# Kernel optimization log

Measured on AMD Instinct MI355X. Metric: run time of the kernel, lower is better.

The kernel has to match this reference:

```python
import jax, jax.numpy as jnp
import numpy as np

B, S, D_MODEL = 4, 2048, 1024
NUM_HEADS, HEAD_DIM = 16, 64
EPS = 1e-6


def setup_inputs() -> dict:
    key = jax.random.key(0)
    ks = jax.random.split(key, 6)
    hd = NUM_HEADS * HEAD_DIM
    scale_in = 1.0 / np.sqrt(D_MODEL)
    scale_hd = 1.0 / np.sqrt(hd)
    return {
        "x": jax.random.normal(ks[0], (B, S, D_MODEL), dtype=jnp.float32),
        "w_q": jax.random.normal(ks[1], (D_MODEL, hd), dtype=jnp.float32) * scale_in,
        "w_k": jax.random.normal(ks[2], (D_MODEL, hd), dtype=jnp.float32) * scale_in,
        "w_v": jax.random.normal(ks[3], (D_MODEL, hd), dtype=jnp.float32) * scale_in,
        "w_proj": jax.random.normal(ks[4], (hd, D_MODEL), dtype=jnp.float32) * scale_hd,
        "b_proj": jax.random.normal(ks[5], (D_MODEL,), dtype=jnp.float32) * 0.01,
        "ln_gamma": jnp.ones((D_MODEL,), dtype=jnp.float32),
        "ln_beta": jnp.zeros((D_MODEL,), dtype=jnp.float32),
    }


def reference(x, w_q, w_k, w_v, w_proj, b_proj, ln_gamma, ln_beta):
    # x: [B, S, D]; project and split heads -> [B, H, S, Dh]
    def split_heads(t):
        b, s, _ = t.shape
        return t.reshape(b, s, NUM_HEADS, HEAD_DIM).transpose(0, 2, 1, 3)

    q = split_heads(x @ w_q)
    k = split_heads(x @ w_k)
    v = split_heads(x @ w_v)

    scale = HEAD_DIM ** (-0.5)
    attn = jnp.einsum("bnqd,bnkd->bnqk", q, k) * scale  # [B, H, S, S]
    attn = jax.nn.softmax(attn, axis=-1)
    o = jnp.einsum("bnqk,bnkd->bnqd", attn, v)  # [B, H, S, Dh]
    o = o.transpose(0, 2, 1, 3).reshape(x.shape[0], x.shape[1], NUM_HEADS * HEAD_DIM)

    # proj + residual (dropout = identity in eval) then LayerNorm(eps=1e-6)
    y = o @ w_proj + b_proj + x
    mean = jnp.mean(y, axis=-1, keepdims=True)
    var = jnp.var(y, axis=-1, keepdims=True)
    y = (y - mean) * jax.lax.rsqrt(var + EPS) * ln_gamma + ln_beta
    return y
```

## Files before the change

### kernel.cpp

```cpp
#include <hip/hip_runtime.h>
#include <hip/hip_fp16.h>


typedef unsigned short u16;
typedef __attribute__((ext_vector_type(8))) u16 u16x8;
typedef __attribute__((ext_vector_type(4))) u16 u16x4;
typedef __attribute__((ext_vector_type(8))) __bf16 bf16x8;
typedef __attribute__((ext_vector_type(4))) _Float16 f16x4;
typedef __attribute__((ext_vector_type(2))) _Float16 f16x2;
typedef __attribute__((ext_vector_type(2))) __fp16 hf16x2;
typedef __attribute__((ext_vector_type(4))) float f32x4;

#define SM_C1 0.1803368801111204f

static __device__ __forceinline__ u16 f2bf(float f) {
  union { float f; unsigned int u; } v; v.f = f;
  unsigned int u = v.u;
  return (u16)((u + 0x7fffu + ((u >> 16) & 1u)) >> 16);
}
static __device__ __forceinline__ u16 f2h(float f) {
  union { _Float16 h; u16 u; } v; v.h = (_Float16)f;
  return v.u;
}

static __device__ __forceinline__ void gld16(const u16* g, u16* l) {
  __builtin_amdgcn_global_load_lds((const __attribute__((address_space(1))) void*)g,
                                   (__attribute__((address_space(3))) void*)l, 16, 0, 0);
}


__global__ __launch_bounds__(256) void k_convx(const float* __restrict__ x,
                                               u16* __restrict__ xbf) {
  int i = (blockIdx.x * 256 + threadIdx.x) * 8;
  float4 a = *(const float4*)(x + i);
  float4 b = *(const float4*)(x + i + 4);
  u16x8 o;
  o[0] = f2bf(a.x); o[1] = f2bf(a.y); o[2] = f2bf(a.z); o[3] = f2bf(a.w);
  o[4] = f2bf(b.x); o[5] = f2bf(b.y); o[6] = f2bf(b.z); o[7] = f2bf(b.w);
  *(u16x8*)(xbf + i) = o;
}

__global__ __launch_bounds__(256) void k_convwT(const float* __restrict__ w0,
                                                const float* __restrict__ w1,
                                                const float* __restrict__ w2,
                                                const float* __restrict__ w3,
                                                u16* __restrict__ o0, u16* __restrict__ o1,
                                                u16* __restrict__ o2, u16* __restrict__ o3) {
  __shared__ float tile[64][65];
  const float* w = blockIdx.z == 0 ? w0 : blockIdx.z == 1 ? w1 : blockIdx.z == 2 ? w2 : w3;
  u16* o = blockIdx.z == 0 ? o0 : blockIdx.z == 1 ? o1 : blockIdx.z == 2 ? o2 : o3;
  const int k0 = blockIdx.x * 64, n0 = blockIdx.y * 64;
  const int t = threadIdx.x;
#pragma unroll
  for (int i = 0; i < 16; i++) {
    int idx = t + 256 * i;
    int k = idx >> 6, n = idx & 63;
    tile[k][n] = w[(k0 + k) * 1024 + n0 + n];
  }
  __syncthreads();
#pragma unroll
  for (int i = 0; i < 16; i++) {
    int idx = t + 256 * i;
    int n = idx >> 6, k = idx & 63;
    o[(n0 + n) * 1024 + k0 + k] = f2bf(tile[k][n]);
  }
}


__global__ __launch_bounds__(256) void k_gemm_qkv(const u16* __restrict__ xbf,
                                                  const u16* __restrict__ wT,
                                                  u16* __restrict__ Qb, u16* __restrict__ Kb,
                                                  u16* __restrict__ VbT) {
  __shared__ alignas(16) u16 Als[128 * 64];
  __shared__ alignas(16) u16 Bls[128 * 64];
  const int t = threadIdx.x;
  const int wv = t >> 6, lane = t & 63, quad = lane >> 4, l16 = lane & 15;
  const int wm = wv >> 1, wn = wv & 1;
  const int m0 = blockIdx.x * 128;
  const int nt = blockIdx.y;
  const int row = t >> 3;
  const int kg = (t & 7) ^ (row & 7);
  const u16* aG = xbf + (size_t)(m0 + row) * 1024 + kg * 8;
  const u16* bG = wT + (size_t)(nt * 128 + row) * 1024 + kg * 8;
  const int sw = l16 & 7;
  const int aA0 = (wm * 64 + l16) * 64 + ((quad) ^ sw) * 8;
  const int aA1 = (wm * 64 + l16) * 64 + ((4 + quad) ^ sw) * 8;
  const int bA0 = (wn * 64 + l16) * 64 + ((quad) ^ sw) * 8;
  const int bA1 = (wn * 64 + l16) * 64 + ((4 + quad) ^ sw) * 8;

  f32x4 acc[4][4] = {};
  for (int k0 = 0; k0 < 1024; k0 += 64) {
    __syncthreads();
#pragma unroll
    for (int i = 0; i < 4; i++) {
      gld16(aG + i * 32 * 1024 + k0, &Als[(i * 256 + wv * 64) * 8]);
      gld16(bG + i * 32 * 1024 + k0, &Bls[(i * 256 + wv * 64) * 8]);
    }
    __syncthreads();
#pragma unroll
    for (int c = 0; c < 2; c++) {
      bf16x8 a[4], b[4];
#pragma unroll
      for (int f = 0; f < 4; f++) a[f] = *(const bf16x8*)&Als[(c ? aA1 : aA0) + f * 1024];
#pragma unroll
      for (int g = 0; g < 4; g++) b[g] = *(const bf16x8*)&Bls[(c ? bA1 : bA0) + g * 1024];
#pragma unroll
      for (int f = 0; f < 4; f++)
#pragma unroll
        for (int g = 0; g < 4; g++)
          acc[f][g] = __builtin_amdgcn_mfma_f32_16x16x32_bf16(a[f], b[g], acc[f][g], 0, 0, 0);
    }
  }

  const int sel = nt >> 3;
  const int n0 = (nt & 7) * 128 + wn * 64;
  const int mBase = m0 + wm * 64 + quad * 4;
  if (sel < 2) {
    u16* Ob = sel == 0 ? Qb : Kb;
    const float scl = sel == 0 ? SM_C1 : 1.0f;
#pragma unroll
    for (int f = 0; f < 4; f++)
#pragma unroll
      for (int g = 0; g < 4; g++)
#pragma unroll
        for (int r = 0; r < 4; r++) {
          int m = mBase + f * 16 + r;
          int n = n0 + g * 16 + l16;
          Ob[(size_t)m * 1024 + n] = f2bf(acc[f][g][r] * scl);
        }
  } else {
#pragma unroll
    for (int f = 0; f < 4; f++) {
      int m = mBase + f * 16;
      int bb = m >> 11, s = m & 2047;
#pragma unroll
      for (int g = 0; g < 4; g++) {
        int n = n0 + g * 16 + l16;
        int hh = n >> 6, dh = n & 63;
        u16x4 o;
#pragma unroll
        for (int r = 0; r < 4; r++) o[r] = f2h(acc[f][g][r]);
        *(u16x4*)&VbT[(size_t)(((bb << 4) + hh) * 64 + dh) * 2048 + s] = o;
      }
    }
  }
}


__global__ __launch_bounds__(256) void k_gemm_proj(const u16* __restrict__ Abf,
                                                   const u16* __restrict__ wT,
                                                   const float* __restrict__ x,
                                                   const float* __restrict__ bias,
                                                   float* __restrict__ ypre) {
  __shared__ alignas(16) u16 Als[128 * 64];
  __shared__ alignas(16) u16 Bls[128 * 64];
  const int t = threadIdx.x;
  const int wv = t >> 6, lane = t & 63, quad = lane >> 4, l16 = lane & 15;
  const int wm = wv >> 1, wn = wv & 1;
  const int m0 = blockIdx.x * 128;
  const int n0t = blockIdx.y * 128;
  const int row = t >> 3;
  const int kg = (t & 7) ^ (row & 7);
  const u16* aG = Abf + (size_t)(m0 + row) * 1024 + kg * 8;
  const u16* bG = wT + (size_t)(n0t + row) * 1024 + kg * 8;
  const int sw = l16 & 7;
  const int aA0 = (wm * 64 + l16) * 64 + ((quad) ^ sw) * 8;
  const int aA1 = (wm * 64 + l16) * 64 + ((4 + quad) ^ sw) * 8;
  const int bA0 = (wn * 64 + l16) * 64 + ((quad) ^ sw) * 8;
  const int bA1 = (wn * 64 + l16) * 64 + ((4 + quad) ^ sw) * 8;

  f32x4 acc[4][4] = {};
  for (int k0 = 0; k0 < 1024; k0 += 64) {
    __syncthreads();
#pragma unroll
    for (int i = 0; i < 4; i++) {
      gld16(aG + i * 32 * 1024 + k0, &Als[(i * 256 + wv * 64) * 8]);
      gld16(bG + i * 32 * 1024 + k0, &Bls[(i * 256 + wv * 64) * 8]);
    }
    __syncthreads();
#pragma unroll
    for (int c = 0; c < 2; c++) {
      bf16x8 a[4], b[4];
#pragma unroll
      for (int f = 0; f < 4; f++) a[f] = *(const bf16x8*)&Als[(c ? aA1 : aA0) + f * 1024];
#pragma unroll
      for (int g = 0; g < 4; g++) b[g] = *(const bf16x8*)&Bls[(c ? bA1 : bA0) + g * 1024];
#pragma unroll
      for (int f = 0; f < 4; f++)
#pragma unroll
        for (int g = 0; g < 4; g++)
          acc[f][g] = __builtin_amdgcn_mfma_f32_16x16x32_bf16(a[f], b[g], acc[f][g], 0, 0, 0);
    }
  }

  const int n0 = n0t + wn * 64;
  const int mBase = m0 + wm * 64 + quad * 4;
#pragma unroll
  for (int g = 0; g < 4; g++) {
    int n = n0 + g * 16 + l16;
    float bn = bias[n];
#pragma unroll
    for (int f = 0; f < 4; f++)
#pragma unroll
      for (int r = 0; r < 4; r++) {
        int m = mBase + f * 16 + r;
        ypre[(size_t)m * 1024 + n] = acc[f][g][r] + bn + x[(size_t)m * 1024 + n];
      }
  }
}


__global__ __launch_bounds__(256) void k_attn(const u16* __restrict__ Qb,
                                              const u16* __restrict__ Kb,
                                              const u16* __restrict__ VbT,
                                              u16* __restrict__ Ob) {
  __shared__ alignas(16) u16 Kls[2][64 * 72];
  __shared__ alignas(16) u16 Vls[2][64 * 72];
  const int b = blockIdx.y >> 4, h = blockIdx.y & 15;
  const int q0 = blockIdx.x * 128;
  const int t = threadIdx.x;
  const int wave = t >> 6, lane = t & 63, quad = lane >> 4, l16 = lane & 15;
  const int sr = t >> 2, sc = (t & 3) * 8;

  bf16x8 aq[2][2];
#pragma unroll
  for (int qf = 0; qf < 2; qf++)
#pragma unroll
    for (int c = 0; c < 2; c++)
      aq[qf][c] = *(const bf16x8*)&Qb[(size_t)(b * 2048 + q0 + wave * 32 + qf * 16 + l16) * 1024 +
                                      h * 64 + c * 32 + quad * 8];

  f32x4 Oacc[2][4] = {};
  float psum[2] = {};

  const u16* kBase = Kb + (size_t)(b * 2048) * 1024 + h * 64;
  const u16* vtRow = VbT + (size_t)((b * 16 + h) * 64 + sr) * 2048;

  u16x8 rk0, rk1, rv0, rv1;
  {
    const u16* kR = kBase + (size_t)sr * 1024;
    rk0 = *(const u16x8*)(kR + sc);
    rk1 = *(const u16x8*)(kR + sc + 32);
    rv0 = *(const u16x8*)(vtRow + sc);
    rv1 = *(const u16x8*)(vtRow + sc + 32);
  }

  for (int kt = 0; kt < 32; kt++) {
    const int p = kt & 1;
    *(u16x8*)&Kls[p][sr * 72 + sc]      = rk0;
    *(u16x8*)&Kls[p][sr * 72 + sc + 32] = rk1;
    *(u16x8*)&Vls[p][sr * 72 + sc]      = rv0;
    *(u16x8*)&Vls[p][sr * 72 + sc + 32] = rv1;
    __syncthreads();
    if (kt < 31) {
      const int kv1 = (kt + 1) * 64;
      const u16* kR = kBase + (size_t)(kv1 + sr) * 1024;
      rk0 = *(const u16x8*)(kR + sc);
      rk1 = *(const u16x8*)(kR + sc + 32);
      rv0 = *(const u16x8*)(vtRow + kv1 + sc);
      rv1 = *(const u16x8*)(vtRow + kv1 + sc + 32);
    }

    f32x4 st[2][4] = {};
#pragma unroll
    for (int c = 0; c < 2; c++) {
      bf16x8 bk[4];
#pragma unroll
      for (int f = 0; f < 4; f++)
        bk[f] = *(const bf16x8*)&Kls[p][(f * 16 + l16) * 72 + c * 32 + quad * 8];
#pragma unroll
      for (int qf = 0; qf < 2; qf++)
#pragma unroll
        for (int f = 0; f < 4; f++)
          st[qf][f] = __builtin_amdgcn_mfma_f32_16x16x32_bf16(bk[f], aq[qf][c], st[qf][f], 0, 0, 0);
    }

#pragma unroll
    for (int qf = 0; qf < 2; qf++) {
      union PK { hf16x2 r; f16x2 v; __half2 h; };
      PK e01[4], e23[4];
      __half2 it2 = __half2{__half(0.f), __half(0.f)};
#pragma unroll
      for (int f = 0; f < 4; f++) {
        PK a01, a23;
        a01.r = __builtin_amdgcn_cvt_pkrtz(st[qf][f][0], st[qf][f][1]);
        a23.r = __builtin_amdgcn_cvt_pkrtz(st[qf][f][2], st[qf][f][3]);
        e01[f].h = h2exp2(a01.h);
        e23[f].h = h2exp2(a23.h);
        it2 = __hadd2(it2, __hadd2(e01[f].h, e23[f].h));
      }
      psum[qf] += __low2float(it2) + __high2float(it2);
#pragma unroll
      for (int f = 0; f < 4; f++) {
        union { f16x4 v; f16x2 h[2]; } pb;
        pb.h[0] = e01[f].v;
        pb.h[1] = e23[f].v;
#pragma unroll
        for (int g = 0; g < 4; g++) {
          f16x4 va = *(const f16x4*)&Vls[p][(g * 16 + l16) * 72 + f * 16 + quad * 4];
          Oacc[qf][g] = __builtin_amdgcn_mfma_f32_16x16x16f16(va, pb.v, Oacc[qf][g], 0, 0, 0);
        }
      }
    }
  }

  float inv[2];
#pragma unroll
  for (int qf = 0; qf < 2; qf++) {
    float v = psum[qf];
    v += __shfl_xor(v, 16);
    v += __shfl_xor(v, 32);
    inv[qf] = 1.f / v;
  }

  __syncthreads();
  u16* Ols = (u16*)Kls;
#pragma unroll
  for (int qf = 0; qf < 2; qf++)
#pragma unroll
    for (int g = 0; g < 4; g++) {
      u16x4 o;
#pragma unroll
      for (int r = 0; r < 4; r++) o[r] = f2bf(Oacc[qf][g][r] * inv[qf]);
      *(u16x4*)&Ols[(wave * 32 + qf * 16 + l16) * 72 + g * 16 + quad * 4] = o;
    }
  __syncthreads();
  const int row = t >> 1, half = t & 1;
  u16* gO = Ob + (size_t)(b * 2048 + q0 + row) * 1024 + h * 64 + half * 32;
#pragma unroll
  for (int j = 0; j < 4; j++)
    *(u16x8*)(gO + j * 8) = *(const u16x8*)&Ols[row * 72 + half * 32 + j * 8];
}


__global__ __launch_bounds__(256) void k_ln(const float* __restrict__ y,
                                            const float* __restrict__ g,
                                            const float* __restrict__ bt,
                                            float* __restrict__ out) {
  const int row = blockIdx.x;
  const int t = threadIdx.x;
  float4 v = *(const float4*)(y + row * 1024 + t * 4);
  float s1 = v.x + v.y + v.z + v.w;
  float s2 = v.x * v.x + v.y * v.y + v.z * v.z + v.w * v.w;
#pragma unroll
  for (int off = 32; off; off >>= 1) {
    s1 += __shfl_down(s1, off);
    s2 += __shfl_down(s2, off);
  }
  __shared__ float red[10];
  const int wave = t >> 6, lane = t & 63;
  if (lane == 0) { red[wave] = s1; red[4 + wave] = s2; }
  __syncthreads();
  if (t == 0) {
    float a = red[0] + red[1] + red[2] + red[3];
    float bsum = red[4] + red[5] + red[6] + red[7];
    float mean = a * (1.f / 1024.f);
    float var = bsum * (1.f / 1024.f) - mean * mean;
    red[8] = mean;
    red[9] = rsqrtf(var + 1e-6f);
  }
  __syncthreads();
  float mean = red[8], iv = red[9];
  float4 gv = *(const float4*)(g + t * 4);
  float4 bv = *(const float4*)(bt + t * 4);
  float4 o;
  o.x = (v.x - mean) * iv * gv.x + bv.x;
  o.y = (v.y - mean) * iv * gv.y + bv.y;
  o.z = (v.z - mean) * iv * gv.z + bv.z;
  o.w = (v.w - mean) * iv * gv.w + bv.w;
  *(float4*)(out + row * 1024 + t * 4) = o;
}


extern "C" void kernel_launch(void* const* d_in, const int* in_sizes, int n_in,
                              void* d_out, int out_size, void* d_ws, size_t ws_size,
                              hipStream_t stream) {
  const float* x  = (const float*)d_in[0];
  const float* wq = (const float*)d_in[1];
  const float* wk = (const float*)d_in[2];
  const float* wv = (const float*)d_in[3];
  const float* wp = (const float*)d_in[4];
  const float* bp = (const float*)d_in[5];
  const float* g  = (const float*)d_in[6];
  const float* bt = (const float*)d_in[7];
  float* out = (float*)d_out;
  char* ws = (char*)d_ws;

  u16* xbf = (u16*)(ws);
  u16* wqT = (u16*)(ws + (16 << 20));
  u16* wkT = wqT + (size_t)1024 * 1024;
  u16* wvT = wqT + (size_t)2048 * 1024;
  u16* wpT = (u16*)(ws + (22 << 20));
  u16* Qb  = (u16*)(ws + (24 << 20));
  u16* Kb  = (u16*)(ws + (40 << 20));
  u16* VbT = (u16*)(ws + (56 << 20));
  u16* Ob  = (u16*)(ws);
  float* ypre = (float*)(ws + (24 << 20));

  k_convx<<<4096, 256, 0, stream>>>(x, xbf);
  k_convwT<<<dim3(16, 16, 4), 256, 0, stream>>>(wq, wk, wv, wp, wqT, wkT, wvT, wpT);
  k_gemm_qkv<<<dim3(64, 24), 256, 0, stream>>>(xbf, wqT, Qb, Kb, VbT);
  k_attn<<<dim3(16, 64), 256, 0, stream>>>(Qb, Kb, VbT, Ob);
  k_gemm_proj<<<dim3(64, 8), 256, 0, stream>>>(Ob, wpT, x, bp, ypre);
  k_ln<<<8192, 256, 0, stream>>>(ypre, g, bt, out);
}
```

Measured before the change: 305.1 us.

## Double attention query tile per block and store pre-LN activations in bf16

The attention kernel now handles 256 query rows per block (64 per wave), so each K/V tile loaded into LDS is reused across twice as many queries. V fragments are hoisted into registers once per tile, and launch bounds request two blocks per CU. Separately, the projection output before LayerNorm is written and read as bf16 instead of fp32, halving that intermediate traffic. The trade-offs are higher register pressure, only 512 attention blocks, and some precision loss in the residual sum feeding LayerNorm.

Measured after the change: 274.5 us. -10.0%, faster.

```diff
diff --git a/kernel.cpp b/kernel.cpp
--- a/kernel.cpp
+++ b/kernel.cpp
@@ -17,6 +17,10 @@
   union { float f; unsigned int u; } v; v.f = f;
   unsigned int u = v.u;
   return (u16)((u + 0x7fffu + ((u >> 16) & 1u)) >> 16);
+}
+static __device__ __forceinline__ float bf2f(u16 b) {
+  union { unsigned int u; float f; } v; v.u = ((unsigned int)b) << 16;
+  return v.f;
 }
 static __device__ __forceinline__ u16 f2h(float f) {
   union { _Float16 h; u16 u; } v; v.h = (_Float16)f;
@@ -151,7 +155,7 @@
                                                    const u16* __restrict__ wT,
                                                    const float* __restrict__ x,
                                                    const float* __restrict__ bias,
-                                                   float* __restrict__ ypre) {
+                                                   u16* __restrict__ ypre) {
   __shared__ alignas(16) u16 Als[128 * 64];
   __shared__ alignas(16) u16 Bls[128 * 64];
   const int t = threadIdx.x;
@@ -204,34 +208,33 @@
 #pragma unroll
       for (int r = 0; r < 4; r++) {
         int m = mBase + f * 16 + r;
-        ypre[(size_t)m * 1024 + n] = acc[f][g][r] + bn + x[(size_t)m * 1024 + n];
+        ypre[(size_t)m * 1024 + n] = f2bf(acc[f][g][r] + bn + x[(size_t)m * 1024 + n]);
       }
   }
 }
 
 
-__global__ __launch_bounds__(256) void k_attn(const u16* __restrict__ Qb,
-                                              const u16* __restrict__ Kb,
-                                              const u16* __restrict__ VbT,
-                                              u16* __restrict__ Ob) {
-  __shared__ alignas(16) u16 Kls[2][64 * 72];
-  __shared__ alignas(16) u16 Vls[2][64 * 72];
+__global__ __launch_bounds__(256, 2) void k_attn(const u16* __restrict__ Qb,
+                                                 const u16* __restrict__ Kb,
+                                                 const u16* __restrict__ VbT,
+                                                 u16* __restrict__ Ob) {
+  __shared__ alignas(16) u16 smem[4][64 * 72];
   const int b = blockIdx.y >> 4, h = blockIdx.y & 15;
-  const int q0 = blockIdx.x * 128;
+  const int q0 = blockIdx.x * 256;
   const int t = threadIdx.x;
   const int wave = t >> 6, lane = t & 63, quad = lane >> 4, l16 = lane & 15;
   const int sr = t >> 2, sc = (t & 3) * 8;
 
-  bf16x8 aq[2][2];
-#pragma unroll
-  for (int qf = 0; qf < 2; qf++)
+  bf16x8 aq[4][2];
+#pragma unroll
+  for (int qf = 0; qf < 4; qf++)
 #pragma unroll
     for (int c = 0; c < 2; c++)
-      aq[qf][c] = *(const bf16x8*)&Qb[(size_t)(b * 2048 + q0 + wave * 32 + qf * 16 + l16) * 1024 +
+      aq[qf][c] = *(const bf16x8*)&Qb[(size_t)(b * 2048 + q0 + wave * 64 + qf * 16 + l16) * 1024 +
                                       h * 64 + c * 32 + quad * 8];
 
-  f32x4 Oacc[2][4] = {};
-  float psum[2] = {};
+  f32x4 Oacc[4][4] = {};
+  float psum[4] = {};
 
   const u16* kBase = Kb + (size_t)(b * 2048) * 1024 + h * 64;
   const u16* vtRow = VbT + (size_t)((b * 16 + h) * 64 + sr) * 2048;
@@ -247,10 +250,12 @@
 
   for (int kt = 0; kt < 32; kt++) {
     const int p = kt & 1;
-    *(u16x8*)&Kls[p][sr * 72 + sc]      = rk0;
-    *(u16x8*)&Kls[p][sr * 72 + sc + 32] = rk1;
-    *(u16x8*)&Vls[p][sr * 72 + sc]      = rv0;
-    *(u16x8*)&Vls[p][sr * 72 + sc + 32] = rv1;
+    u16* Kls = smem[p];
+    u16* Vls = smem[2 + p];
+    *(u16x8*)&Kls[sr * 72 + sc]      = rk0;
+    *(u16x8*)&Kls[sr * 72 + sc + 32] = rk1;
+    *(u16x8*)&Vls[sr * 72 + sc]      = rv0;
+    *(u16x8*)&Vls[sr * 72 + sc + 32] = rv1;
     __syncthreads();
     if (kt < 31) {
       const int kv1 = (kt + 1) * 64;
@@ -261,22 +266,33 @@
       rv1 = *(const u16x8*)(vtRow + kv1 + sc + 32);
     }
 
-    f32x4 st[2][4] = {};
+    f32x4 st[4][4];
+#pragma unroll
+    for (int qf = 0; qf < 4; qf++)
+#pragma unroll
+      for (int f = 0; f < 4; f++) st[qf][f] = f32x4{0.f, 0.f, 0.f, 0.f};
 #pragma unroll
     for (int c = 0; c < 2; c++) {
       bf16x8 bk[4];
 #pragma unroll
       for (int f = 0; f < 4; f++)
-        bk[f] = *(const bf16x8*)&Kls[p][(f * 16 + l16) * 72 + c * 32 + quad * 8];
-#pragma unroll
-      for (int qf = 0; qf < 2; qf++)
+        bk[f] = *(const bf16x8*)&Kls[(f * 16 + l16) * 72 + c * 32 + quad * 8];
+#pragma unroll
+      for (int qf = 0; qf < 4; qf++)
 #pragma unroll
         for (int f = 0; f < 4; f++)
           st[qf][f] = __builtin_amdgcn_mfma_f32_16x16x32_bf16(bk[f], aq[qf][c], st[qf][f], 0, 0, 0);
     }
 
-#pragma unroll
-    for (int qf = 0; qf < 2; qf++) {
+    f16x4 va[4][4];
+#pragma unroll
+    for (int f = 0; f < 4; f++)
+#pragma unroll
+      for (int g = 0; g < 4; g++)
+        va[f][g] = *(const f16x4*)&Vls[(g * 16 + l16) * 72 + f * 16 + quad * 4];
+
+#pragma unroll
+    for (int qf = 0; qf < 4; qf++) {
       union PK { hf16x2 r; f16x2 v; __half2 h; };
       PK e01[4], e23[4];
       __half2 it2 = __half2{__half(0.f), __half(0.f)};
@@ -296,17 +312,15 @@
         pb.h[0] = e01[f].v;
         pb.h[1] = e23[f].v;
 #pragma unroll
-        for (int g = 0; g < 4; g++) {
-          f16x4 va = *(const f16x4*)&Vls[p][(g * 16 + l16) * 72 + f * 16 + quad * 4];
-          Oacc[qf][g] = __builtin_amdgcn_mfma_f32_16x16x16f16(va, pb.v, Oacc[qf][g], 0, 0, 0);
-        }
+        for (int g = 0; g < 4; g++)
+          Oacc[qf][g] = __builtin_amdgcn_mfma_f32_16x16x16f16(va[f][g], pb.v, Oacc[qf][g], 0, 0, 0);
       }
     }
   }
 
-  float inv[2];
-#pragma unroll
-  for (int qf = 0; qf < 2; qf++) {
+  float inv[4];
+#pragma unroll
+  for (int qf = 0; qf < 4; qf++) {
     float v = psum[qf];
     v += __shfl_xor(v, 16);
     v += __shfl_xor(v, 32);
@@ -314,34 +328,34 @@
   }
 
   __syncthreads();
-  u16* Ols = (u16*)Kls;
-#pragma unroll
-  for (int qf = 0; qf < 2; qf++)
+  u16* Ols = (u16*)smem;
+#pragma unroll
+  for (int qf = 0; qf < 4; qf++)
 #pragma unroll
     for (int g = 0; g < 4; g++) {
       u16x4 o;
 #pragma unroll
       for (int r = 0; r < 4; r++) o[r] = f2bf(Oacc[qf][g][r] * inv[qf]);
-      *(u16x4*)&Ols[(wave * 32 + qf * 16 + l16) * 72 + g * 16 + quad * 4] = o;
+      *(u16x4*)&Ols[(wave * 64 + qf * 16 + l16) * 72 + g * 16 + quad * 4] = o;
     }
   __syncthreads();
-  const int row = t >> 1, half = t & 1;
-  u16* gO = Ob + (size_t)(b * 2048 + q0 + row) * 1024 + h * 64 + half * 32;
-#pragma unroll
-  for (int j = 0; j < 4; j++)
-    *(u16x8*)(gO + j * 8) = *(const u16x8*)&Ols[row * 72 + half * 32 + j * 8];
-}
-
-
-__global__ __launch_bounds__(256) void k_ln(const float* __restrict__ y,
+  u16* gO = Ob + (size_t)(b * 2048 + q0 + t) * 1024 + h * 64;
+#pragma unroll
+  for (int j = 0; j < 8; j++)
+    *(u16x8*)(gO + j * 8) = *(const u16x8*)&Ols[t * 72 + j * 8];
+}
+
+
+__global__ __launch_bounds__(256) void k_ln(const u16* __restrict__ y,
                                             const float* __restrict__ g,
                                             const float* __restrict__ bt,
                                             float* __restrict__ out) {
   const int row = blockIdx.x;
   const int t = threadIdx.x;
-  float4 v = *(const float4*)(y + row * 1024 + t * 4);
-  float s1 = v.x + v.y + v.z + v.w;
-  float s2 = v.x * v.x + v.y * v.y + v.z * v.z + v.w * v.w;
+  u16x4 rv = *(const u16x4*)(y + row * 1024 + t * 4);
+  float vx = bf2f(rv[0]), vy = bf2f(rv[1]), vz = bf2f(rv[2]), vw = bf2f(rv[3]);
+  float s1 = vx + vy + vz + vw;
+  float s2 = vx * vx + vy * vy + vz * vz + vw * vw;
 #pragma unroll
   for (int off = 32; off; off >>= 1) {
     s1 += __shfl_down(s1, off);
@@ -364,10 +378,10 @@
   float4 gv = *(const float4*)(g + t * 4);
   float4 bv = *(const float4*)(bt + t * 4);
   float4 o;
-  o.x = (v.x - mean) * iv * gv.x + bv.x;
-  o.y = (v.y - mean) * iv * gv.y + bv.y;
-  o.z = (v.z - mean) * iv * gv.z + bv.z;
-  o.w = (v.w - mean) * iv * gv.w + bv.w;
+  o.x = (vx - mean) * iv * gv.x + bv.x;
+  o.y = (vy - mean) * iv * gv.y + bv.y;
+  o.z = (vz - mean) * iv * gv.z + bv.z;
+  o.w = (vw - mean) * iv * gv.w + bv.w;
   *(float4*)(out + row * 1024 + t * 4) = o;
 }
 
@@ -395,12 +409,12 @@
   u16* Kb  = (u16*)(ws + (40 << 20));
   u16* VbT = (u16*)(ws + (56 << 20));
   u16* Ob  = (u16*)(ws);
-  float* ypre = (float*)(ws + (24 << 20));
+  u16* ypre = (u16*)(ws + (24 << 20));
 
   k_convx<<<4096, 256, 0, stream>>>(x, xbf);
   k_convwT<<<dim3(16, 16, 4), 256, 0, stream>>>(wq, wk, wv, wp, wqT, wkT, wvT, wpT);
   k_gemm_qkv<<<dim3(64, 24), 256, 0, stream>>>(xbf, wqT, Qb, Kb, VbT);
-  k_attn<<<dim3(16, 64), 256, 0, stream>>>(Qb, Kb, VbT, Ob);
+  k_attn<<<dim3(8, 64), 256, 0, stream>>>(Qb, Kb, VbT, Ob);
   k_gemm_proj<<<dim3(64, 8), 256, 0, stream>>>(Ob, wpT, x, bp, ypre);
   k_ln<<<8192, 256, 0, stream>>>(ypre, g, bt, out);
 }
```
